# Optimization experiments

Hardware: AMD Instinct MI355X
Metric: run time of the kernel (lower is better)

The kernel has to match this reference:

```python
import jax, jax.numpy as jnp
import numpy as np

IMAGE_DIM = (1000, 1000)   # (width, height) as used by the torch module
PATCH_SIZE = 5
NUM_TERMS = 10
NUM_PATCHES = (IMAGE_DIM[0] // PATCH_SIZE) * (IMAGE_DIM[1] // PATCH_SIZE)


def setup_inputs() -> dict:
    key = jax.random.key(0)
    k1, k2 = jax.random.split(key, 2)
    num_pixels = IMAGE_DIM[0] * IMAGE_DIM[1]
    pix_coord = jax.random.uniform(k1, (num_pixels, 2), dtype=jnp.float32)
    # xavier_uniform on [num_patches, 3, num_terms, 2]: fan_in=num_terms, fan_out=2 (last two dims)
    bound = float(np.sqrt(6.0 / (NUM_TERMS + 2)))
    coefficients = jax.random.uniform(
        k2, (NUM_PATCHES, 3, NUM_TERMS, 2), dtype=jnp.float32,
        minval=-bound, maxval=bound)
    bias = jnp.zeros((NUM_PATCHES, 3), dtype=jnp.float32)
    return {"pix_coord": pix_coord, "coefficients": coefficients, "bias": bias}


def reference(pix_coord, coefficients, bias):
    width = IMAGE_DIM[0]
    num_pixels = pix_coord.shape[0]
    idx = jnp.arange(num_pixels, dtype=jnp.int32)
    row = idx // width
    col = idx % width
    patch_idx = (row // PATCH_SIZE) * (width // PATCH_SIZE) + col // PATCH_SIZE  # [N]
    powers = jnp.arange(NUM_TERMS, dtype=jnp.float32)                            # [T]
    # Vandermonde in each coordinate: [N, 2, T]
    vand = pix_coord[:, :, None] ** powers
    cg = coefficients[patch_idx]   # [N, 3, T, 2]
    bg = bias[patch_idx]           # [N, 3]
    # sum_d sum_t coeff[n,c,t,d] * pix[n,d]^t  + bias  -> output [3, N]
    out = jnp.einsum('nctd,ndt->cn', cg, vand) + bg.T
    return out
```

## Files before the change

kernel.cpp:

```cpp
#include <hip/hip_runtime.h>

constexpr int WIDTH     = 1000;
constexpr int HEIGHT    = 1000;
constexpr int N_PIXELS  = WIDTH * HEIGHT;
constexpr int PATCH     = 5;
constexpr int PATCHES_X = WIDTH / PATCH;
constexpr int BLOCK     = 256;
constexpr int MAXP      = BLOCK / PATCH + 2;

__global__ __launch_bounds__(256) void ts_approx_kernel(
    const float* __restrict__ pix,
    const float* __restrict__ coef,
    const float* __restrict__ bias,
    float* __restrict__ out)
{
    __shared__ float scoef[MAXP * 60];
    __shared__ float sbias[MAXP * 3];

    const int tid  = threadIdx.x;
    const int row  = blockIdx.y;
    const int c0   = blockIdx.x * BLOCK;
    const int prow = row / PATCH;
    const int p0   = c0 / PATCH;
    const int pend = min(c0 + BLOCK - 1, WIDTH - 1) / PATCH;
    const int np   = pend - p0 + 1;

    const float4* g4 = reinterpret_cast<const float4*>(coef + (size_t)(prow * PATCHES_X + p0) * 60);
    float4* s4 = reinterpret_cast<float4*>(scoef);
    const int nf4 = np * 15;
    for (int j = tid; j < nf4; j += BLOCK) s4[j] = g4[j];

    const float* gb = bias + (size_t)(prow * PATCHES_X + p0) * 3;
    for (int j = tid; j < np * 3; j += BLOCK) sbias[j] = gb[j];

    __syncthreads();

    const int col = c0 + tid;
    if (col >= WIDTH) return;
    const int n = row * WIDTH + col;

    const float2 p = reinterpret_cast<const float2*>(pix)[n];
    const float x = p.x, y = p.y;

    const int pl = col / PATCH - p0;
    const float4* c4 = reinterpret_cast<const float4*>(scoef + pl * 60);
    float a0 = sbias[pl * 3 + 0];
    float a1 = sbias[pl * 3 + 1];
    float a2 = sbias[pl * 3 + 2];

    float xt = 1.0f, yt = 1.0f;
    #pragma unroll
    for (int i = 0; i < 5; ++i) {
        const float xt1 = xt * x, yt1 = yt * y;
        const float4 v0 = c4[i];
        a0 = fmaf(v0.x, xt,  a0); a0 = fmaf(v0.y, yt,  a0);
        a0 = fmaf(v0.z, xt1, a0); a0 = fmaf(v0.w, yt1, a0);
        const float4 v1 = c4[5 + i];
        a1 = fmaf(v1.x, xt,  a1); a1 = fmaf(v1.y, yt,  a1);
        a1 = fmaf(v1.z, xt1, a1); a1 = fmaf(v1.w, yt1, a1);
        const float4 v2 = c4[10 + i];
        a2 = fmaf(v2.x, xt,  a2); a2 = fmaf(v2.y, yt,  a2);
        a2 = fmaf(v2.z, xt1, a2); a2 = fmaf(v2.w, yt1, a2);
        xt = xt1 * x; yt = yt1 * y;
    }

    out[0 * N_PIXELS + n] = a0;
    out[1 * N_PIXELS + n] = a1;
    out[2 * N_PIXELS + n] = a2;
}

extern "C" void kernel_launch(void* const* d_in, const int* in_sizes, int n_in,
                              void* d_out, int out_size, void* d_ws, size_t ws_size,
                              hipStream_t stream) {
    const float* pix  = (const float*)d_in[0];
    const float* coef = (const float*)d_in[1];
    const float* bias = (const float*)d_in[2];
    float* out = (float*)d_out;

    dim3 grid((WIDTH + BLOCK - 1) / BLOCK, HEIGHT);
    ts_approx_kernel<<<grid, BLOCK, 0, stream>>>(pix, coef, bias, out);
}
```

Baseline: 13.12 us.

## Process a full patch row per block, reusing register-held coefficients across rows

Each block now covers one patch row (five image rows) rather than a single pixel row, so the grid shrinks by a factor of five. Each thread loads its patch's 60 coefficients from shared memory into registers once and reuses them for five pixels. This is meant to cut the redundant global-to-shared coefficient loads (each patch was reloaded five times) and the per-pixel shared reads. In exchange it raises register pressure (about 60 extra VGPRs) and reduces the number of blocks to 800, which may lower occupancy and latency hiding.

```diff
diff --git a/kernel.cpp b/kernel.cpp
--- a/kernel.cpp
+++ b/kernel.cpp
@@ -18,9 +18,8 @@
     __shared__ float sbias[MAXP * 3];
 
     const int tid  = threadIdx.x;
-    const int row  = blockIdx.y;
+    const int prow = blockIdx.y;
     const int c0   = blockIdx.x * BLOCK;
-    const int prow = row / PATCH;
     const int p0   = c0 / PATCH;
     const int pend = min(c0 + BLOCK - 1, WIDTH - 1) / PATCH;
     const int np   = pend - p0 + 1;
@@ -29,44 +28,53 @@
     float4* s4 = reinterpret_cast<float4*>(scoef);
     const int nf4 = np * 15;
     for (int j = tid; j < nf4; j += BLOCK) s4[j] = g4[j];
-
     const float* gb = bias + (size_t)(prow * PATCHES_X + p0) * 3;
     for (int j = tid; j < np * 3; j += BLOCK) sbias[j] = gb[j];
-
     __syncthreads();
 
     const int col = c0 + tid;
     if (col >= WIDTH) return;
-    const int n = row * WIDTH + col;
 
-    const float2 p = reinterpret_cast<const float2*>(pix)[n];
-    const float x = p.x, y = p.y;
+    const int row0 = prow * PATCH;
+    const int pl   = col / PATCH - p0;
 
-    const int pl = col / PATCH - p0;
+    float4 cf[15];
     const float4* c4 = reinterpret_cast<const float4*>(scoef + pl * 60);
-    float a0 = sbias[pl * 3 + 0];
-    float a1 = sbias[pl * 3 + 1];
-    float a2 = sbias[pl * 3 + 2];
+    #pragma unroll
+    for (int i = 0; i < 15; ++i) cf[i] = c4[i];
+    const float b0 = sbias[pl * 3 + 0];
+    const float b1 = sbias[pl * 3 + 1];
+    const float b2 = sbias[pl * 3 + 2];
 
-    float xt = 1.0f, yt = 1.0f;
+    const float2* p2 = reinterpret_cast<const float2*>(pix);
+
     #pragma unroll
-    for (int i = 0; i < 5; ++i) {
-        const float xt1 = xt * x, yt1 = yt * y;
-        const float4 v0 = c4[i];
-        a0 = fmaf(v0.x, xt,  a0); a0 = fmaf(v0.y, yt,  a0);
-        a0 = fmaf(v0.z, xt1, a0); a0 = fmaf(v0.w, yt1, a0);
-        const float4 v1 = c4[5 + i];
-        a1 = fmaf(v1.x, xt,  a1); a1 = fmaf(v1.y, yt,  a1);
-        a1 = fmaf(v1.z, xt1, a1); a1 = fmaf(v1.w, yt1, a1);
-        const float4 v2 = c4[10 + i];
-        a2 = fmaf(v2.x, xt,  a2); a2 = fmaf(v2.y, yt,  a2);
-        a2 = fmaf(v2.z, xt1, a2); a2 = fmaf(v2.w, yt1, a2);
-        xt = xt1 * x; yt = yt1 * y;
+    for (int r = 0; r < PATCH; ++r) {
+        const int n = (row0 + r) * WIDTH + col;
+        const float2 p = p2[n];
+        const float x = p.x, y = p.y;
+
+        float a0 = b0, a1 = b1, a2 = b2;
+        float xt = 1.0f, yt = 1.0f;
+        #pragma unroll
+        for (int i = 0; i < 5; ++i) {
+            const float xt1 = xt * x, yt1 = yt * y;
+            float4 v = cf[i];
+            a0 = fmaf(v.x, xt,  a0); a0 = fmaf(v.y, yt,  a0);
+            a0 = fmaf(v.z, xt1, a0); a0 = fmaf(v.w, yt1, a0);
+            v = cf[5 + i];
+            a1 = fmaf(v.x, xt,  a1); a1 = fmaf(v.y, yt,  a1);
+            a1 = fmaf(v.z, xt1, a1); a1 = fmaf(v.w, yt1, a1);
+            v = cf[10 + i];
+            a2 = fmaf(v.x, xt,  a2); a2 = fmaf(v.y, yt,  a2);
+            a2 = fmaf(v.z, xt1, a2); a2 = fmaf(v.w, yt1, a2);
+            xt = xt1 * x; yt = yt1 * y;
+        }
+
+        out[0 * N_PIXELS + n] = a0;
+        out[1 * N_PIXELS + n] = a1;
+        out[2 * N_PIXELS + n] = a2;
     }
-
-    out[0 * N_PIXELS + n] = a0;
-    out[1 * N_PIXELS + n] = a1;
-    out[2 * N_PIXELS + n] = a2;
 }
 
 extern "C" void kernel_launch(void* const* d_in, const int* in_sizes, int n_in,
@@ -77,6 +85,6 @@
     const float* bias = (const float*)d_in[2];
     float* out = (float*)d_out;
 
-    dim3 grid((WIDTH + BLOCK - 1) / BLOCK, HEIGHT);
+    dim3 grid((WIDTH + BLOCK - 1) / BLOCK, HEIGHT / PATCH);
     ts_approx_kernel<<<grid, BLOCK, 0, stream>>>(pix, coef, bias, out);
 }
```

Result: faster. 11.72 us (-10.7%).
